# Kernel tuning notes

Hardware: AMD Instinct MI355X
Metric: run time of the kernel (lower is better)

The kernel has to match this reference:

```python
import jax, jax.numpy as jnp
import numpy as np


def _rbf(x, z):
    # x: [..., M, D], z: [N, D] or [..., K, D] -> pairwise exp(-0.5*||x-z||^2)
    x2 = jnp.sum(x * x, axis=-1)[..., :, None]
    z2 = jnp.sum(z * z, axis=-1)[..., None, :]
    xz = jnp.einsum('...md,...nd->...mn', x, z)
    sq = jnp.maximum(x2 + z2 - 2.0 * xz, 0.0)
    return jnp.exp(-0.5 * sq)


def setup_inputs() -> dict:
    key = jax.random.key(0)
    k1, k2, k3, k4, k5 = jax.random.split(key, 5)
    B, M, P, N = 8, 1024, 256, 4096
    X = jax.random.normal(k1, (B, M, P), dtype=jnp.float32)
    A = jax.random.randint(k2, (B, M), 0, 2, dtype=jnp.int32)
    XA_train = jax.random.normal(k3, (N, P + 1), dtype=jnp.float32)
    alpha = jax.random.normal(k4, (N,), dtype=jnp.float32)
    K_inv = jax.random.normal(k5, (N, N), dtype=jnp.float32) * 0.01
    return {"X": X, "A": A, "XA_train": XA_train, "alpha": alpha, "K_inv": K_inv}


def reference(X, A, XA_train, alpha, K_inv):
    # XA = concat([X, A[..., None]])  -> [B, M, P+1]
    XA = jnp.concatenate([X, A.astype(X.dtype)[..., None]], axis=-1)
    # kernel(XA, XA_train): [B, M, N]
    Kxz = _rbf(XA, XA_train)
    # f_loc = einsum('...mn,...n->...m', K(XA, train), alpha)
    f_loc = jnp.einsum('bmn,n->bm', Kxz, alpha)
    # kernel(XA_train, XA) == Kxz^T for a symmetric kernel
    Kzx = jnp.swapaxes(Kxz, -1, -2)  # [B, N, M]
    # cov_train_x = K_inv @ K(train, XA): [B, N, M]
    cov_train_x = jnp.einsum('tn,bnk->btk', K_inv, Kzx)
    # f_cov = K(XA, XA) - K(XA, train) @ cov_train_x: [B, M, M]
    Kxx = _rbf(XA, XA)
    f_cov = Kxx - jnp.einsum('bmn,bnk->bmk', Kxz, cov_train_x)
    f_var = jnp.diagonal(f_cov, axis1=-2, axis2=-1)  # [B, M]
    return f_loc, f_var
```

## Files before the change

### kernel.cpp

```cpp
#include <hip/hip_runtime.h>
#include <math.h>

#define R_ROWS 8192
#define NP     4096
#define DREAL  257
#define DPAD   256

#define BM 128
#define BN 128
#define BK 32
#define LDSS 32
#define NBLKX (R_ROWS / BM)
#define NBLKY (NP / BN)

using frag8 = __attribute__((ext_vector_type(8))) short;
using f32x4 = __attribute__((ext_vector_type(4))) float;

static __device__ __forceinline__ float bf2f(unsigned short u) {
    return __uint_as_float(((unsigned int)u) << 16);
}
static __device__ __forceinline__ unsigned short f2bf(float f) {
    unsigned int u = __float_as_uint(f);
    unsigned int lsb = (u >> 16) & 1u;
    u += 0x7fffu + lsb;
    return (unsigned short)(u >> 16);
}

static __device__ __forceinline__ void gll16(const unsigned short* g, unsigned short* l) {
    __builtin_amdgcn_global_load_lds(
        (const __attribute__((address_space(1))) unsigned int*)g,
        (__attribute__((address_space(3))) unsigned int*)l, 16, 0, 0);
}

__global__ void prep_all(const float* __restrict__ X, const int* __restrict__ A,
                         const float* __restrict__ Z,
                         unsigned short* __restrict__ XAb, unsigned short* __restrict__ Zb,
                         float* __restrict__ x2, float* __restrict__ z2,
                         float* __restrict__ zlast, float* __restrict__ af,
                         char* __restrict__ flags,
                         float* __restrict__ out) {
    int b = blockIdx.x;
    int tid = threadIdx.x;
    if (b < 3) {
        int off = b * 4096 + tid * 16;
        uint4 zz = {0, 0, 0, 0};
        if (off < 8448) *(uint4*)(flags + off) = zz;
    } else if (b < 11) {
        int off = (b - 3) * 1024 + tid * 4;
        float4 zz4 = {0.f, 0.f, 0.f, 0.f};
        *(float4*)(out + off) = zz4;
    } else if (b < 19) {
        int off = R_ROWS + (b - 11) * 1024 + tid * 4;
        float4 oo = {1.f, 1.f, 1.f, 1.f};
        *(float4*)(out + off) = oo;
    }

    int row  = b * 4 + (tid >> 6);
    int lane = tid & 63;
    float s = 0.f;
    if (row < R_ROWS) {
        const float* xr = X + (size_t)row * 256;
        unsigned short* o = XAb + (size_t)row * 256;
#pragma unroll
        for (int i = 0; i < 4; i++) {
            float v = xr[lane + 64 * i];
            s += v * v;
            o[lane + 64 * i] = f2bf(v);
        }
        if (lane == 0) {
            float a = (float)A[row];
            af[row] = a;
            s += a * a;
        }
#pragma unroll
        for (int off = 32; off; off >>= 1) s += __shfl_down(s, off, 64);
        if (lane == 0) x2[row] = s;
    } else {
        int zi = row - R_ROWS;
        if (zi >= NP) return;
        const float* zr = Z + (size_t)zi * DREAL;
        unsigned short* o = Zb + (size_t)zi * 256;
#pragma unroll
        for (int i = 0; i < 4; i++) {
            float v = zr[lane + 64 * i];
            s += v * v;
            o[lane + 64 * i] = f2bf(v);
        }
        if (lane == 0) {
            float v = zr[256];
            s += v * v;
            zlast[zi] = bf2f(f2bf(v));
        }
#pragma unroll
        for (int off = 32; off; off >>= 1) s += __shfl_down(s, off, 64);
        if (lane == 0) z2[zi] = s;
    }
}

__global__ __launch_bounds__(256, 2) void gemm_kxz(
    const unsigned short* __restrict__ Abuf,
    const unsigned short* __restrict__ Bbuf,
    const float* __restrict__ x2, const float* __restrict__ z2,
    const float* __restrict__ zlast, const float* __restrict__ af,
    const float* __restrict__ alpha,
    unsigned short* __restrict__ Kb,
    float* __restrict__ floc_out,
    int* __restrict__ rowflag, int* __restrict__ tileflag)
{
    __shared__ unsigned short sh[2][4][BM * LDSS];
    const int m0 = blockIdx.x * BM, n0 = blockIdx.y * BN;
    const int tid = threadIdx.x, lane = tid & 63, wave = tid >> 6;
    const int wr = wave >> 1, wc = wave & 1;
    const int q = lane >> 4, rr = lane & 15;
    const int grow = lane >> 2, gcol = (lane & 3) * 8;

    f32x4 acc[4][4] = {};
#pragma unroll
    for (int ph = 0; ph < 2; ph++) {
        int k0 = ph * 128;
#pragma unroll
        for (int s3 = 0; s3 < 4; s3++) {
            int ks = k0 + s3 * BK;
#pragma unroll
            for (int c = 0; c < 2; c++) {
                int r = wave * 32 + c * 16 + grow;
                gll16(Abuf + (size_t)(m0 + r) * 256 + ks + gcol,
                      &sh[0][s3][(wave * 32 + c * 16) * LDSS]);
                gll16(Bbuf + (size_t)(n0 + r) * 256 + ks + gcol,
                      &sh[1][s3][(wave * 32 + c * 16) * LDSS]);
            }
        }
        __syncthreads();
#pragma unroll
        for (int s3 = 0; s3 < 4; s3++) {
            frag8 afr[4], bfr[4];
#pragma unroll
            for (int i = 0; i < 4; i++) {
                afr[i] = *(const frag8*)(&sh[0][s3][(wr * 64 + i * 16 + rr) * LDSS + q * 8]);
                bfr[i] = *(const frag8*)(&sh[1][s3][(wc * 64 + i * 16 + rr) * LDSS + q * 8]);
            }
#pragma unroll
            for (int i = 0; i < 4; i++)
#pragma unroll
                for (int j = 0; j < 4; j++)
                    acc[i][j] = __builtin_amdgcn_mfma_f32_16x16x32_bf16(afr[i], bfr[j], acc[i][j], 0, 0, 0);
        }
        __syncthreads();
    }
    float zn[4], zl[4];
#pragma unroll
    for (int j = 0; j < 4; j++) {
        int n = n0 + wc * 64 + j * 16 + rr;
        zn[j] = z2[n];
        zl[j] = zlast[n];
    }
    bool anyl = false;
#pragma unroll
    for (int i = 0; i < 4; i++)
#pragma unroll
        for (int reg = 0; reg < 4; reg++) {
            int ml = wr * 64 + i * 16 + q * 4 + reg;
            float x  = x2[m0 + ml];
            float am = af[m0 + ml];
#pragma unroll
            for (int j = 0; j < 4; j++) {
                float xz = fmaf(am, zl[j], acc[i][j][reg]);
                float d = x + zn[j] - 2.0f * xz;
                anyl |= !(d >= 186.0f);
            }
        }
    unsigned long long wb = __ballot(anyl);
    int* sflag = (int*)&sh[0][0][0];
    if (lane == 0) sflag[wave] = (wb != 0ULL) ? 1 : 0;
    __syncthreads();
    if (sflag[0] | sflag[1] | sflag[2] | sflag[3]) {
        float av[4];
#pragma unroll
        for (int j = 0; j < 4; j++) av[j] = alpha[n0 + wc * 64 + j * 16 + rr];
        unsigned int wany = 0;
#pragma unroll
        for (int i = 0; i < 4; i++) {
#pragma unroll
            for (int reg = 0; reg < 4; reg++) {
                int ml = wr * 64 + i * 16 + q * 4 + reg;
                float x  = x2[m0 + ml];
                float am = af[m0 + ml];
                float s = 0.f;
#pragma unroll
                for (int j = 0; j < 4; j++) {
                    float xz = fmaf(am, zl[j], acc[i][j][reg]);
                    float d = fmaxf(x + zn[j] - 2.0f * xz, 0.0f);
                    unsigned short bv = f2bf(__expf(-0.5f * d));
                    wany |= bv;
                    Kb[(size_t)(m0 + ml) * NP + n0 + wc * 64 + j * 16 + rr] = bv;
                    s += bf2f(bv) * av[j];
                }
                s += __shfl_xor(s, 1, 64);
                s += __shfl_xor(s, 2, 64);
                s += __shfl_xor(s, 4, 64);
                s += __shfl_xor(s, 8, 64);
                if (rr == 0 && s != 0.0f) atomicAdd(&floc_out[m0 + ml], s);
            }
        }
        unsigned long long b2 = __ballot(wany != 0);
        if (lane == 0 && b2 != 0ULL) {
            atomicOr(&tileflag[blockIdx.x * NBLKY + blockIdx.y], 1);
            atomicOr(&rowflag[blockIdx.x], 1);
        }
    }
}

__global__ __launch_bounds__(256, 4) void gemm_q(
    const unsigned short* __restrict__ Kb,
    const float* __restrict__ Kinv,
    float* __restrict__ out,
    const int* __restrict__ rowflag, const int* __restrict__ tileflag)
{
    const int m0 = blockIdx.x * BM, t0 = blockIdx.y * BN;
    if (rowflag[blockIdx.x] == 0) return;

    __shared__ unsigned short sA[BM * LDSS];
    __shared__ unsigned short sB[BN * LDSS];
    const int tid = threadIdx.x, lane = tid & 63, wave = tid >> 6;
    const int wr = wave >> 1, wc = wave & 1;
    const int q = lane >> 4, rr = lane & 15;
    const int grow = lane >> 2, gcol = (lane & 3) * 8;
    const int mblk = blockIdx.x * NBLKY;

    f32x4 acc[4][4] = {};
    for (int kb = 0; kb < NBLKY; kb++) {
        if (tileflag[mblk + kb] == 0) continue;
        int kk0 = kb * BN;
#pragma unroll
        for (int k2 = 0; k2 < BN; k2 += BK) {
            int kk = kk0 + k2;
#pragma unroll
            for (int c = 0; c < 2; c++) {
                int rl = wave * 32 + c * 16 + grow;
                gll16(Kb + (size_t)(m0 + rl) * NP + kk + gcol,
                      &sA[(wave * 32 + c * 16) * LDSS]);
                const float* gp = Kinv + (size_t)(t0 + rl) * NP + kk + gcol;
                float4 v0 = *(const float4*)gp;
                float4 v1 = *(const float4*)(gp + 4);
                unsigned short tmp[8];
                tmp[0] = f2bf(v0.x); tmp[1] = f2bf(v0.y);
                tmp[2] = f2bf(v0.z); tmp[3] = f2bf(v0.w);
                tmp[4] = f2bf(v1.x); tmp[5] = f2bf(v1.y);
                tmp[6] = f2bf(v1.z); tmp[7] = f2bf(v1.w);
                *(uint4*)(&sB[rl * LDSS + gcol]) = *(const uint4*)tmp;
            }
            __syncthreads();
            frag8 afr[4], bfr[4];
#pragma unroll
            for (int i = 0; i < 4; i++) {
                afr[i] = *(const frag8*)(&sA[(wr * 64 + i * 16 + rr) * LDSS + q * 8]);
                bfr[i] = *(const frag8*)(&sB[(wc * 64 + i * 16 + rr) * LDSS + q * 8]);
            }
#pragma unroll
            for (int i = 0; i < 4; i++)
#pragma unroll
                for (int j = 0; j < 4; j++)
                    acc[i][j] = __builtin_amdgcn_mfma_f32_16x16x32_bf16(afr[i], bfr[j], acc[i][j], 0, 0, 0);
            __syncthreads();
        }
    }
    if (tileflag[mblk + blockIdx.y] == 0) return;
#pragma unroll
    for (int i = 0; i < 4; i++) {
#pragma unroll
        for (int reg = 0; reg < 4; reg++) {
            int m = m0 + wr * 64 + i * 16 + q * 4 + reg;
            float s = 0.f;
#pragma unroll
            for (int j = 0; j < 4; j++) {
                int t = t0 + wc * 64 + j * 16 + rr;
                s += acc[i][j][reg] * bf2f(Kb[(size_t)m * NP + t]);
            }
            s += __shfl_xor(s, 1, 64);
            s += __shfl_xor(s, 2, 64);
            s += __shfl_xor(s, 4, 64);
            s += __shfl_xor(s, 8, 64);
            if (rr == 0 && s != 0.0f) atomicAdd(&out[R_ROWS + m], -s);
        }
    }
}

extern "C" void kernel_launch(void* const* d_in, const int* in_sizes, int n_in,
                              void* d_out, int out_size, void* d_ws, size_t ws_size,
                              hipStream_t stream) {
    const float* X     = (const float*)d_in[0];
    const int*   A     = (const int*)d_in[1];
    const float* Z     = (const float*)d_in[2];
    const float* alpha = (const float*)d_in[3];
    const float* Kinv  = (const float*)d_in[4];
    float* out = (float*)d_out;

    char* ws = (char*)d_ws;
    unsigned short* XAb = (unsigned short*)(ws);
    unsigned short* Zb  = (unsigned short*)(ws + 4194304);
    float* x2    = (float*)(ws + 6291456);
    float* z2    = (float*)(ws + 6324224);
    float* zlast = (float*)(ws + 6340608);
    float* af    = (float*)(ws + 6356992);
    int*   rowflag  = (int*)(ws + 6389760);
    int*   tileflag = (int*)(ws + 6390016);
    unsigned short* Kb = (unsigned short*)(ws + 6398208);

    prep_all<<<(R_ROWS + NP) / 4, 256, 0, stream>>>(X, A, Z, XAb, Zb, x2, z2, zlast, af,
                                                    (char*)rowflag, out);
    gemm_kxz<<<dim3(NBLKX, NBLKY), 256, 0, stream>>>(XAb, Zb, x2, z2, zlast, af, alpha,
                                                     Kb, out, rowflag, tileflag);
    gemm_q<<<dim3(NBLKX, NBLKY), 256, 0, stream>>>(Kb, Kinv, out, rowflag, tileflag);
}
```

Measured before the change: 127.9 us.

## Enlarge Kxz GEMM tile to 256 rows and vectorize prep loads

The Kxz GEMM tile grows from 128x128 to 256x128, so each wave holds an 8x4 accumulator block. The K loop is restructured into four phases of 64 with smaller LDS buffers. Tile and row flags are now kept at 256-row granularity, and gemm_q maps its 128-row blocks onto them. This aims to reuse B fragments more and halve the number of blocks, at the cost of higher register pressure and coarser skip granularity in gemm_q. The prep kernel also switches to float4/ushort4 accesses, which changes the element-to-lane mapping.

```diff
diff --git a/kernel.cpp b/kernel.cpp
--- a/kernel.cpp
+++ b/kernel.cpp
@@ -4,14 +4,14 @@
 #define R_ROWS 8192
 #define NP     4096
 #define DREAL  257
-#define DPAD   256
-
-#define BM 128
+#define KDIM   256
+
+#define BM 256
 #define BN 128
 #define BK 32
 #define LDSS 32
-#define NBLKX (R_ROWS / BM)
-#define NBLKY (NP / BN)
+#define MB256 (R_ROWS / BM)
+#define NB128 (NP / BN)
 
 using frag8 = __attribute__((ext_vector_type(8))) short;
 using f32x4 = __attribute__((ext_vector_type(4))) float;
@@ -61,12 +61,10 @@
     if (row < R_ROWS) {
         const float* xr = X + (size_t)row * 256;
         unsigned short* o = XAb + (size_t)row * 256;
-#pragma unroll
-        for (int i = 0; i < 4; i++) {
-            float v = xr[lane + 64 * i];
-            s += v * v;
-            o[lane + 64 * i] = f2bf(v);
-        }
+        float4 v = *(const float4*)(xr + lane * 4);
+        s = v.x * v.x + v.y * v.y + v.z * v.z + v.w * v.w;
+        ushort4 p = {f2bf(v.x), f2bf(v.y), f2bf(v.z), f2bf(v.w)};
+        *(ushort4*)(o + lane * 4) = p;
         if (lane == 0) {
             float a = (float)A[row];
             af[row] = a;
@@ -80,16 +78,16 @@
         if (zi >= NP) return;
         const float* zr = Z + (size_t)zi * DREAL;
         unsigned short* o = Zb + (size_t)zi * 256;
-#pragma unroll
-        for (int i = 0; i < 4; i++) {
-            float v = zr[lane + 64 * i];
-            s += v * v;
-            o[lane + 64 * i] = f2bf(v);
-        }
+        float4 v;
+        v.x = zr[lane * 4 + 0]; v.y = zr[lane * 4 + 1];
+        v.z = zr[lane * 4 + 2]; v.w = zr[lane * 4 + 3];
+        s = v.x * v.x + v.y * v.y + v.z * v.z + v.w * v.w;
+        ushort4 p = {f2bf(v.x), f2bf(v.y), f2bf(v.z), f2bf(v.w)};
+        *(ushort4*)(o + lane * 4) = p;
         if (lane == 0) {
-            float v = zr[256];
-            s += v * v;
-            zlast[zi] = bf2f(f2bf(v));
+            float v256 = zr[256];
+            s += v256 * v256;
+            zlast[zi] = bf2f(f2bf(v256));
         }
 #pragma unroll
         for (int off = 32; off; off >>= 1) s += __shfl_down(s, off, 64);
@@ -107,40 +105,47 @@
     float* __restrict__ floc_out,
     int* __restrict__ rowflag, int* __restrict__ tileflag)
 {
-    __shared__ unsigned short sh[2][4][BM * LDSS];
+    __shared__ unsigned short sA[2][BM * LDSS];
+    __shared__ unsigned short sB[2][BN * LDSS];
+    __shared__ int sflag[4];
     const int m0 = blockIdx.x * BM, n0 = blockIdx.y * BN;
     const int tid = threadIdx.x, lane = tid & 63, wave = tid >> 6;
     const int wr = wave >> 1, wc = wave & 1;
     const int q = lane >> 4, rr = lane & 15;
     const int grow = lane >> 2, gcol = (lane & 3) * 8;
 
-    f32x4 acc[4][4] = {};
-#pragma unroll
-    for (int ph = 0; ph < 2; ph++) {
-        int k0 = ph * 128;
-#pragma unroll
-        for (int s3 = 0; s3 < 4; s3++) {
-            int ks = k0 + s3 * BK;
+    f32x4 acc[8][4] = {};
+#pragma unroll
+    for (int ph = 0; ph < 4; ph++) {
+        int k0 = ph * 64;
+#pragma unroll
+        for (int s2 = 0; s2 < 2; s2++) {
+            int ks = k0 + s2 * BK;
+#pragma unroll
+            for (int c = 0; c < 4; c++) {
+                int r = wave * 64 + c * 16 + grow;
+                gll16(Abuf + (size_t)(m0 + r) * 256 + ks + gcol,
+                      &sA[s2][(wave * 64 + c * 16) * LDSS]);
+            }
 #pragma unroll
             for (int c = 0; c < 2; c++) {
                 int r = wave * 32 + c * 16 + grow;
-                gll16(Abuf + (size_t)(m0 + r) * 256 + ks + gcol,
-                      &sh[0][s3][(wave * 32 + c * 16) * LDSS]);
                 gll16(Bbuf + (size_t)(n0 + r) * 256 + ks + gcol,
-                      &sh[1][s3][(wave * 32 + c * 16) * LDSS]);
+                      &sB[s2][(wave * 32 + c * 16) * LDSS]);
             }
         }
         __syncthreads();
 #pragma unroll
-        for (int s3 = 0; s3 < 4; s3++) {
-            frag8 afr[4], bfr[4];
-#pragma unroll
-            for (int i = 0; i < 4; i++) {
-                afr[i] = *(const frag8*)(&sh[0][s3][(wr * 64 + i * 16 + rr) * LDSS + q * 8]);
-                bfr[i] = *(const frag8*)(&sh[1][s3][(wc * 64 + i * 16 + rr) * LDSS + q * 8]);
-            }
-#pragma unroll
-            for (int i = 0; i < 4; i++)
+        for (int s2 = 0; s2 < 2; s2++) {
+            frag8 afr[8], bfr[4];
+#pragma unroll
+            for (int i = 0; i < 8; i++)
+                afr[i] = *(const frag8*)(&sA[s2][(wr * 128 + i * 16 + rr) * LDSS + q * 8]);
+#pragma unroll
+            for (int j = 0; j < 4; j++)
+                bfr[j] = *(const frag8*)(&sB[s2][(wc * 64 + j * 16 + rr) * LDSS + q * 8]);
+#pragma unroll
+            for (int i = 0; i < 8; i++)
 #pragma unroll
                 for (int j = 0; j < 4; j++)
                     acc[i][j] = __builtin_amdgcn_mfma_f32_16x16x32_bf16(afr[i], bfr[j], acc[i][j], 0, 0, 0);
@@ -156,10 +161,10 @@
     }
     bool anyl = false;
 #pragma unroll
-    for (int i = 0; i < 4; i++)
+    for (int i = 0; i < 8; i++)
 #pragma unroll
         for (int reg = 0; reg < 4; reg++) {
-            int ml = wr * 64 + i * 16 + q * 4 + reg;
+            int ml = wr * 128 + i * 16 + q * 4 + reg;
             float x  = x2[m0 + ml];
             float am = af[m0 + ml];
 #pragma unroll
@@ -170,7 +175,6 @@
             }
         }
     unsigned long long wb = __ballot(anyl);
-    int* sflag = (int*)&sh[0][0][0];
     if (lane == 0) sflag[wave] = (wb != 0ULL) ? 1 : 0;
     __syncthreads();
     if (sflag[0] | sflag[1] | sflag[2] | sflag[3]) {
@@ -179,10 +183,10 @@
         for (int j = 0; j < 4; j++) av[j] = alpha[n0 + wc * 64 + j * 16 + rr];
         unsigned int wany = 0;
 #pragma unroll
-        for (int i = 0; i < 4; i++) {
+        for (int i = 0; i < 8; i++) {
 #pragma unroll
             for (int reg = 0; reg < 4; reg++) {
-                int ml = wr * 64 + i * 16 + q * 4 + reg;
+                int ml = wr * 128 + i * 16 + q * 4 + reg;
                 float x  = x2[m0 + ml];
                 float am = af[m0 + ml];
                 float s = 0.f;
@@ -204,7 +208,7 @@
         }
         unsigned long long b2 = __ballot(wany != 0);
         if (lane == 0 && b2 != 0ULL) {
-            atomicOr(&tileflag[blockIdx.x * NBLKY + blockIdx.y], 1);
+            atomicOr(&tileflag[blockIdx.x * NB128 + blockIdx.y], 1);
             atomicOr(&rowflag[blockIdx.x], 1);
         }
     }
@@ -216,20 +220,20 @@
     float* __restrict__ out,
     const int* __restrict__ rowflag, const int* __restrict__ tileflag)
 {
-    const int m0 = blockIdx.x * BM, t0 = blockIdx.y * BN;
-    if (rowflag[blockIdx.x] == 0) return;
-
-    __shared__ unsigned short sA[BM * LDSS];
+    const int mrow = blockIdx.x >> 1;
+    if (rowflag[mrow] == 0) return;
+    const int m0 = blockIdx.x * 128, t0 = blockIdx.y * BN;
+
+    __shared__ unsigned short sA[128 * LDSS];
     __shared__ unsigned short sB[BN * LDSS];
     const int tid = threadIdx.x, lane = tid & 63, wave = tid >> 6;
     const int wr = wave >> 1, wc = wave & 1;
     const int q = lane >> 4, rr = lane & 15;
     const int grow = lane >> 2, gcol = (lane & 3) * 8;
-    const int mblk = blockIdx.x * NBLKY;
 
     f32x4 acc[4][4] = {};
-    for (int kb = 0; kb < NBLKY; kb++) {
-        if (tileflag[mblk + kb] == 0) continue;
+    for (int kb = 0; kb < NB128; kb++) {
+        if (tileflag[mrow * NB128 + kb] == 0) continue;
         int kk0 = kb * BN;
 #pragma unroll
         for (int k2 = 0; k2 < BN; k2 += BK) {
@@ -264,7 +268,7 @@
             __syncthreads();
         }
     }
-    if (tileflag[mblk + blockIdx.y] == 0) return;
+    if (tileflag[mrow * NB128 + blockIdx.y] == 0) return;
 #pragma unroll
     for (int i = 0; i < 4; i++) {
 #pragma unroll
@@ -308,7 +312,7 @@
 
     prep_all<<<(R_ROWS + NP) / 4, 256, 0, stream>>>(X, A, Z, XAb, Zb, x2, z2, zlast, af,
                                                     (char*)rowflag, out);
-    gemm_kxz<<<dim3(NBLKX, NBLKY), 256, 0, stream>>>(XAb, Zb, x2, z2, zlast, af, alpha,
+    gemm_kxz<<<dim3(MB256, NB128), 256, 0, stream>>>(XAb, Zb, x2, z2, zlast, af, alpha,
                                                      Kb, out, rowflag, tileflag);
-    gemm_q<<<dim3(NBLKX, NBLKY), 256, 0, stream>>>(Kb, Kinv, out, rowflag, tileflag);
-}
+    gemm_q<<<dim3(R_ROWS / 128, NB128), 256, 0, stream>>>(Kb, Kinv, out, rowflag, tileflag);
+}
```

Result: no change. 126.5 us (-1.1%).
